# Kernel tuning notes

Measured on AMD Instinct MI355X. Metric: run time of the kernel, lower is better.

The kernel has to match this reference:

```python
import jax, jax.numpy as jnp
import numpy as np

GAMMA_NEG = 4.0
GAMMA_POS = 1.0
CLIP = 0.05
EPS = 1e-08
ALPHA3 = 2.0
TOPK = 10
B, C = 4096, 9605


def setup_inputs() -> dict:
    key = jax.random.key(0)
    k1, k2, k3, k4, k5, k6 = jax.random.split(key, 6)
    x = jax.random.normal(k1, (B, C), dtype=jnp.float32)
    y = (jax.random.uniform(k2, (B, C)) < 0.02).astype(jnp.float32)
    whitelist_mask = jax.random.randint(k3, (C,), 0, 100) == 0
    compost_idx = jax.random.randint(k4, (70,), 0, C, dtype=jnp.int32)
    recycle_idx = jax.random.randint(k5, (70,), 0, C, dtype=jnp.int32)
    donate_idx = jax.random.randint(k6, (70,), 0, C, dtype=jnp.int32)
    return {"x": x, "y": y, "whitelist_mask": whitelist_mask,
            "compost_idx": compost_idx, "recycle_idx": recycle_idx,
            "donate_idx": donate_idx}


def reference(x, y, whitelist_mask, compost_idx, recycle_idx, donate_idx):
    xs_pos = jax.nn.sigmoid(x)                       # [B, C]
    xs_neg = jnp.minimum(1.0 - xs_pos + CLIP, 1.0)   # asymmetric clipping
    # base binary cross-entropy (positive log term, clamped)
    loss = (y * jnp.log(jnp.maximum(xs_pos, EPS))
            + (1.0 - y) * jnp.log(jnp.maximum(xs_neg, EPS)))

    # per-sample: does ground truth hit any whitelist (compost/recycle/donate)?
    wl_idx = jnp.concatenate([compost_idx, recycle_idx, donate_idx])  # [210]
    gt_none = jnp.sum(y[:, wl_idx], axis=1) == 0.0    # [B] -> gt_whitelist == [4]

    # top-10 predictions per sample (argsort descending, first 10)
    _, top10 = jax.lax.top_k(xs_pos, TOPK)            # [B, 10]
    y_top = jnp.take_along_axis(y, top10, axis=1)     # [B, 10]
    wl_top = whitelist_mask[top10]                    # [B, 10]
    # non-whitelisted class: penalize iff gt hits no whitelist
    # whitelisted class:     penalize iff y[i, index] == 0
    penalize = jnp.where(wl_top, y_top == 0.0, gt_none[:, None])  # [B, 10]
    mult_vals = jnp.where(penalize, ALPHA3, 1.0)      # [B, 10]
    rows = jnp.arange(x.shape[0])[:, None]
    mult = jnp.ones_like(loss).at[rows, top10].set(mult_vals)
    loss = loss * mult

    # asymmetric focal weighting (no grad through the weight)
    pt = xs_pos * y + xs_neg * (1.0 - y)
    one_sided_gamma = GAMMA_POS * y + GAMMA_NEG * (1.0 - y)
    one_sided_w = jax.lax.stop_gradient(jnp.power(1.0 - pt, one_sided_gamma))
    loss = loss * one_sided_w
    return -jnp.sum(loss)
```

## Files before the change

### kernel.cpp

```cpp
#include <hip/hip_runtime.h>
#include <stdint.h>

#define B_DIM 4096
#define C_DIM 9605
#define NT 512
#define NW (NT / 64)
#define TOPK_N 10
#define CAP 1024
#define LOG2E_F 1.4426950408889634f
#define LN2_D 0.6931471805599453
#define CLIP_F 0.05f
#define XTHRESH 2.5f

typedef float f4a __attribute__((ext_vector_type(4), aligned(16)));

__device__ __forceinline__ float sigmoid_f(float x) {
  float e = __builtin_amdgcn_exp2f(-x * LOG2E_F);
  return __builtin_amdgcn_rcpf(1.0f + e);
}

__device__ __forceinline__ float loss2_term(float s, bool pos) {
  float xn = fminf(1.0f + CLIP_F - s, 1.0f);
  float z = pos ? s : xn;
  float logz = __builtin_amdgcn_logf(z);
  float t = fmaxf(s - CLIP_F, 0.0f);
  float t2 = t * t;
  float w = pos ? (1.0f - s) : (t2 * t2);
  return logz * w;
}

__device__ __forceinline__ unsigned long long make_key(float s, int c, bool pos) {
  return ((unsigned long long)__float_as_uint(s) << 15)
       | (unsigned long long)(((uint32_t)(c ^ 0x3FFF) << 1) | (pos ? 1u : 0u));
}

__device__ __forceinline__ void process_elem(float xval, float yval, int c,
                                             float& lsum,
                                             unsigned long long* cand, int* cnt) {
  float s = sigmoid_f(xval);
  bool pos = (yval != 0.0f);
  lsum += loss2_term(s, pos);
  if (xval > XTHRESH) {
    int slot = atomicAdd(cnt, 1);
    if (slot < CAP) cand[slot] = make_key(s, c, pos);
  }
}

__device__ __forceinline__ void process4(const f4a xv, const f4a yv, int cb,
                                         bool active, float& lsum,
                                         unsigned long long* cand, int* cnt) {
  float sv[4], l = 0.0f;
#pragma unroll
  for (int j = 0; j < 4; ++j) {
    sv[j] = sigmoid_f(xv[j]);
    l += loss2_term(sv[j], yv[j] != 0.0f);
  }
  if (active) lsum += l;
  float mx = fmaxf(fmaxf(xv[0], xv[1]), fmaxf(xv[2], xv[3]));
  if (active && mx > XTHRESH) {
#pragma unroll
    for (int j = 0; j < 4; ++j)
      if (xv[j] > XTHRESH) {
        int slot = atomicAdd(cnt, 1);
        if (slot < CAP) cand[slot] = make_key(sv[j], cb + j, yv[j] != 0.0f);
      }
  }
}

__global__ __launch_bounds__(NT, 4) void asym_loss_row_kernel(
    const float* __restrict__ x, const float* __restrict__ y,
    const unsigned char* __restrict__ wl_mask,
    const int* __restrict__ compost, const int* __restrict__ recycle,
    const int* __restrict__ donate, float* __restrict__ row_out) {
  __shared__ unsigned long long cand[CAP];
  __shared__ float s_part[NW];
  __shared__ int s_cnt;
  __shared__ int s_gtany;

  const int row = blockIdx.x;
  const int tid = threadIdx.x;
  const int lane = tid & 63;
  const int wid = tid >> 6;
  const float* xr = x + (size_t)row * C_DIM;
  const float* yr = y + (size_t)row * C_DIM;

  if (tid == 0) { s_cnt = 0; s_gtany = 0; }
  __syncthreads();

  const int a = (4 - (row & 3)) & 3;
  const float* xa = xr + a;
  const float* ya = yr + a;
  const int Tend = (C_DIM - a - 4) & ~3;

  float ywl = 0.0f;
  if (tid < 210) {
    int idx = (tid < 70) ? compost[tid]
            : (tid < 140) ? recycle[tid - 70]
                          : donate[tid - 140];
    ywl = yr[idx];
  }

  f4a X[5], Y[5];
  int c4t = 4 * NT * 4 + 4 * tid;
  const bool tact = (c4t <= Tend);
  if (!tact) c4t = Tend;
#pragma unroll
  for (int k = 0; k < 4; ++k) {
    int c4 = (k * NT + tid) * 4;
    X[k] = *(const f4a*)(xa + c4);
    Y[k] = *(const f4a*)(ya + c4);
  }
  X[4] = *(const f4a*)(xa + c4t);
  Y[4] = *(const f4a*)(ya + c4t);

  asm volatile("" : "+v"(X[0]), "+v"(X[1]), "+v"(X[2]), "+v"(X[3]), "+v"(X[4]),
                    "+v"(Y[0]), "+v"(Y[1]), "+v"(Y[2]), "+v"(Y[3]), "+v"(Y[4]));

  if (ywl != 0.0f) atomicOr(&s_gtany, 1);

  float lsum = 0.0f;
  if (tid < a) process_elem(xr[tid], yr[tid], tid, lsum, cand, &s_cnt);
#pragma unroll
  for (int k = 0; k < 4; ++k)
    process4(X[k], Y[k], a + (k * NT + tid) * 4, true, lsum, cand, &s_cnt);
  process4(X[4], Y[4], a + c4t, tact, lsum, cand, &s_cnt);
  for (int c = a + Tend + 4 + tid; c < C_DIM; c += NT)
    process_elem(xr[c], yr[c], c, lsum, cand, &s_cnt);

#pragma unroll
  for (int off = 32; off; off >>= 1) lsum += __shfl_xor(lsum, off, 64);
  if (lane == 0) s_part[wid] = lsum;
  __syncthreads();

  if (wid == 0) {
    const int n = s_cnt;
    const bool gt_none = (s_gtany == 0);
    unsigned long long prev = ~0ull;
    unsigned long long mykey = 0ull;

    if (n >= TOPK_N && n <= CAP) {
#pragma unroll 1
      for (int r = 0; r < TOPK_N; ++r) {
        unsigned long long loc = 0ull;
        for (int i = lane; i < n; i += 64) {
          unsigned long long k = cand[i];
          if (k < prev && k > loc) loc = k;
        }
#pragma unroll
        for (int off = 32; off; off >>= 1) {
          unsigned long long o = __shfl_xor(loc, off, 64);
          loc = loc > o ? loc : o;
        }
        if (lane == r) mykey = loc;
        prev = loc;
      }
    } else {
#pragma unroll 1
      for (int r = 0; r < TOPK_N; ++r) {
        unsigned long long loc = 0ull;
        for (int i = lane; i < C_DIM; i += 64) {
          float s = sigmoid_f(xr[i]);
          unsigned long long k = make_key(s, i, yr[i] != 0.0f);
          if (k < prev && k > loc) loc = k;
        }
#pragma unroll
        for (int off = 32; off; off >>= 1) {
          unsigned long long o = __shfl_xor(loc, off, 64);
          loc = loc > o ? loc : o;
        }
        if (lane == r) mykey = loc;
        prev = loc;
      }
    }

    float extra = 0.0f;
    if (lane < TOPK_N) {
      int wc = 0x3FFF ^ (int)((mykey >> 1) & 0x3FFFull);
      bool ypos = (mykey & 1ull) != 0ull;
      float s = __uint_as_float((uint32_t)(mykey >> 15));
      bool wl = (wl_mask[wc] != 0);
      bool pen = wl ? (!ypos) : gt_none;
      if (pen) extra = loss2_term(s, ypos);
    }
#pragma unroll
    for (int off = 32; off; off >>= 1) extra += __shfl_xor(extra, off, 64);
    if (lane == 0) {
      float tot = extra;
#pragma unroll
      for (int w2 = 0; w2 < NW; ++w2) tot += s_part[w2];
      row_out[row] = tot;
    }
  }
}

__global__ void finalize_kernel(const float* __restrict__ row_out,
                                float* __restrict__ out) {
  const int tid = threadIdx.x;
  const int lane = tid & 63;
  const int wid = tid >> 6;
  __shared__ double sp[4];
  double acc = 0.0;
  for (int i = tid; i < B_DIM; i += 256) acc += (double)row_out[i];
#pragma unroll
  for (int off = 32; off; off >>= 1) acc += __shfl_down(acc, off, 64);
  if (lane == 0) sp[wid] = acc;
  __syncthreads();
  if (tid == 0) {
    double t = sp[0] + sp[1] + sp[2] + sp[3];
    out[0] = (float)(-t * LN2_D);
  }
}

extern "C" void kernel_launch(void* const* d_in, const int* in_sizes, int n_in,
                              void* d_out, int out_size, void* d_ws, size_t ws_size,
                              hipStream_t stream) {
  (void)in_sizes; (void)n_in; (void)out_size; (void)ws_size;
  const float* x = (const float*)d_in[0];
  const float* y = (const float*)d_in[1];
  const unsigned char* wl = (const unsigned char*)d_in[2];
  const int* compost = (const int*)d_in[3];
  const int* recycle = (const int*)d_in[4];
  const int* donate  = (const int*)d_in[5];
  float* row_part = (float*)d_ws;

  asym_loss_row_kernel<<<B_DIM, NT, 0, stream>>>(x, y, wl, compost, recycle,
                                                 donate, row_part);
  finalize_kernel<<<1, 256, 0, stream>>>(row_part, (float*)d_out);
}
```

Before: 63.82 us.

## Stream row chunks into LDS via double-buffered global_load_lds

Each row used to be loaded entirely into registers up front. Now it is staged in 2048-element chunks into LDS with asynchronous global_load_lds, using two buffers and vmcnt waits, so loading one chunk overlaps the compute on the other. The candidate buffer shrinks from 1024 to 256 entries and the launch bound asks for 8 blocks per CU, both aimed at cutting register and LDS pressure to raise occupancy. The cost is an extra round trip through LDS for every element and partial serialisation on the waits. The added LDS use (about 34KB per block) may also cap residency below what the launch bound requests.

```diff
diff --git a/kernel.cpp b/kernel.cpp
--- a/kernel.cpp
+++ b/kernel.cpp
@@ -5,14 +5,24 @@
 #define C_DIM 9605
 #define NT 512
 #define NW (NT / 64)
+#define CH 2048
 #define TOPK_N 10
-#define CAP 1024
+#define CAP 256
 #define LOG2E_F 1.4426950408889634f
 #define LN2_D 0.6931471805599453
 #define CLIP_F 0.05f
 #define XTHRESH 2.5f
 
 typedef float f4a __attribute__((ext_vector_type(4), aligned(16)));
+
+__device__ __forceinline__ void gll16(const float* g, float* l) {
+  __builtin_amdgcn_global_load_lds(
+      (const __attribute__((address_space(1))) void*)g,
+      (__attribute__((address_space(3))) void*)(uintptr_t)(void*)l,
+      16, 0, 0);
+}
+
+#define WAITCNT(n) asm volatile("s_waitcnt vmcnt(" #n ")" ::: "memory")
 
 __device__ __forceinline__ float sigmoid_f(float x) {
   float e = __builtin_amdgcn_exp2f(-x * LOG2E_F);
@@ -67,11 +77,13 @@
   }
 }
 
-__global__ __launch_bounds__(NT, 4) void asym_loss_row_kernel(
+__global__ __launch_bounds__(NT, 8) void asym_loss_row_kernel(
     const float* __restrict__ x, const float* __restrict__ y,
     const unsigned char* __restrict__ wl_mask,
     const int* __restrict__ compost, const int* __restrict__ recycle,
     const int* __restrict__ donate, float* __restrict__ row_out) {
+  __shared__ float xbuf[2][CH];
+  __shared__ float ybuf[2][CH];
   __shared__ unsigned long long cand[CAP];
   __shared__ float s_part[NW];
   __shared__ int s_cnt;
@@ -90,7 +102,7 @@
   const int a = (4 - (row & 3)) & 3;
   const float* xa = xr + a;
   const float* ya = yr + a;
-  const int Tend = (C_DIM - a - 4) & ~3;
+  const int elim = (C_DIM - a - 4) & ~3;
 
   float ywl = 0.0f;
   if (tid < 210) {
@@ -100,31 +112,36 @@
     ywl = yr[idx];
   }
 
-  f4a X[5], Y[5];
-  int c4t = 4 * NT * 4 + 4 * tid;
-  const bool tact = (c4t <= Tend);
-  if (!tact) c4t = Tend;
-#pragma unroll
-  for (int k = 0; k < 4; ++k) {
-    int c4 = (k * NT + tid) * 4;
-    X[k] = *(const f4a*)(xa + c4);
-    Y[k] = *(const f4a*)(ya + c4);
-  }
-  X[4] = *(const f4a*)(xa + c4t);
-  Y[4] = *(const f4a*)(ya + c4t);
-
-  asm volatile("" : "+v"(X[0]), "+v"(X[1]), "+v"(X[2]), "+v"(X[3]), "+v"(X[4]),
-                    "+v"(Y[0]), "+v"(Y[1]), "+v"(Y[2]), "+v"(Y[3]), "+v"(Y[4]));
-
+  const int eme = tid * 4;
+#define STAGE(buf, cb) do {                                                  \
+    int e_ = (cb) + eme; e_ = e_ < elim ? e_ : elim;                         \
+    gll16(xa + e_, &xbuf[buf][eme]);                                         \
+    gll16(ya + e_, &ybuf[buf][eme]);                                         \
+  } while (0)
+
+  float lsum = 0.0f;
+#define COMPUTE(buf, cb) do {                                                \
+    int e_ = (cb) + eme;                                                     \
+    bool act_ = (e_ <= elim);                                                \
+    f4a xv_ = *(const f4a*)(&xbuf[buf][eme]);                                \
+    f4a yv_ = *(const f4a*)(&ybuf[buf][eme]);                                \
+    process4(xv_, yv_, a + e_, act_, lsum, cand, &s_cnt);                    \
+  } while (0)
+
+  STAGE(0, 0);
+  STAGE(1, CH);
   if (ywl != 0.0f) atomicOr(&s_gtany, 1);
-
-  float lsum = 0.0f;
+  WAITCNT(2); COMPUTE(0, 0);
+  STAGE(0, 2 * CH);
+  WAITCNT(2); COMPUTE(1, CH);
+  STAGE(1, 3 * CH);
+  WAITCNT(2); COMPUTE(0, 2 * CH);
+  STAGE(0, 4 * CH);
+  WAITCNT(2); COMPUTE(1, 3 * CH);
+  WAITCNT(0); COMPUTE(0, 4 * CH);
+
   if (tid < a) process_elem(xr[tid], yr[tid], tid, lsum, cand, &s_cnt);
-#pragma unroll
-  for (int k = 0; k < 4; ++k)
-    process4(X[k], Y[k], a + (k * NT + tid) * 4, true, lsum, cand, &s_cnt);
-  process4(X[4], Y[4], a + c4t, tact, lsum, cand, &s_cnt);
-  for (int c = a + Tend + 4 + tid; c < C_DIM; c += NT)
+  for (int c = a + elim + 4 + tid; c < C_DIM; c += NT)
     process_elem(xr[c], yr[c], c, lsum, cand, &s_cnt);
 
 #pragma unroll
```

After: 73.52 us. +15.2%, slower.
